# Kernel optimization log

Hardware: AMD Instinct MI355X
Metric: run time of the kernel (lower is better)

## Reference

```python
import jax, jax.numpy as jnp
import numpy as np

B = 8192
K = 64
GLOBAL = 16384  # static size of global index space (fill_max of teacher_indices)
TEMPERATURE = 2.0


def setup_inputs() -> dict:
    key = jax.random.key(0)
    k1, k2, k3 = jax.random.split(key, 3)
    student_logits = jax.random.normal(k1, (B, B), dtype=jnp.float32)
    teacher_scores = jax.random.uniform(k2, (B, K), dtype=jnp.float32)
    batch_indices = jnp.arange(B, dtype=jnp.int32)
    teacher_indices = jax.random.randint(k3, (B, K), 0, GLOBAL, dtype=jnp.int32)
    return {
        "student_logits": student_logits,
        "teacher_scores": teacher_scores,
        "batch_indices": batch_indices,
        "teacher_indices": teacher_indices,
    }


def reference(student_logits, teacher_scores, batch_indices, teacher_indices):
    b = student_logits.shape[0]
    # global -> local mapping table (-1 = not in batch). Static size GLOBAL.
    g2l = jnp.full((GLOBAL,), -1, dtype=jnp.int32).at[batch_indices].set(
        jnp.arange(b, dtype=jnp.int32))
    clamped = jnp.clip(teacher_indices, 0, GLOBAL - 1)
    local_pos = g2l[clamped]                       # [B, K]
    valid = local_pos >= 0
    # invalid entries -> column index b, dropped by scatter mode='drop'
    cols = jnp.where(valid, local_pos, b)
    rows = jnp.broadcast_to(jnp.arange(b, dtype=jnp.int32)[:, None], cols.shape)
    target_probs = jnp.zeros((b, b), dtype=student_logits.dtype)
    target_probs = target_probs.at[rows, cols].set(teacher_scores, mode="drop")
    diag = jnp.arange(b)
    target_probs = target_probs.at[diag, diag].set(1.0)
    row_sums = jnp.clip(target_probs.sum(axis=1, keepdims=True), 1e-8, None)
    target_probs = target_probs / row_sums
    student_log_probs = jax.nn.log_softmax(student_logits / TEMPERATURE, axis=1)
    # KLDivLoss(reduction='batchmean'): sum_t t*(log t - logp) / B, 0 where t==0
    safe_log_t = jnp.log(jnp.where(target_probs > 0, target_probs, 1.0))
    pointwise = jnp.where(target_probs > 0,
                          target_probs * (safe_log_t - student_log_probs), 0.0)
    loss = pointwise.sum() / b
    return loss * (TEMPERATURE ** 2)
```

## Files before the change

### kernel.cpp

```cpp
#include <hip/hip_runtime.h>
#include <math.h>

#define NB 8192
#define NK 64
#define NGLOBAL 16384
#define INV_T 0.5f
#define C_EXP2 0.72134752044448170f

#if defined(__has_builtin)
#if __has_builtin(__builtin_amdgcn_exp2f)
#define EXP2(x) __builtin_amdgcn_exp2f(x)
#endif
#endif
#ifndef EXP2
#define EXP2(x) exp2f(x)
#endif


__global__ __launch_bounds__(256) void row_loss_kernel(
    const float* __restrict__ S,
    const float* __restrict__ tscore,
    const int* __restrict__ tindex,
    const int* __restrict__ bidx,
    float* __restrict__ row_out)
{
    const int row = blockIdx.x;
    const int t = threadIdx.x;
    const float* __restrict__ Srow = S + (size_t)row * NB;
    const float4* rp = reinterpret_cast<const float4*>(Srow);

    float4 v[8];
#pragma unroll
    for (int i = 0; i < 8; ++i) v[i] = rp[i * 256 + t];

    int gi = 0; float sc = 0.f;
    if (t < NK) {
        gi = tindex[(size_t)row * NK + t];
        sc = tscore[(size_t)row * NK + t];
    }

    asm volatile("" ::: "memory");

    float s0 = 0.f, s1 = 0.f, s2 = 0.f, s3 = 0.f;
#pragma unroll
    for (int i = 0; i < 8; ++i) {
        s0 += EXP2(v[i].x * C_EXP2);
        s1 += EXP2(v[i].y * C_EXP2);
        s2 += EXP2(v[i].z * C_EXP2);
        s3 += EXP2(v[i].w * C_EXP2);
    }
    float s = (s0 + s1) + (s2 + s3);
#pragma unroll
    for (int off = 32; off >= 1; off >>= 1) s += __shfl_xor(s, off);
    __shared__ float sred[4];
    if ((t & 63) == 0) sred[t >> 6] = s;
    __syncthreads();

    if (t >= NK) return;

    gi = min(max(gi, 0), NGLOBAL - 1);
    const int col_s = min(gi, NB - 1);
    float gl_spec = Srow[col_s];
    float gd      = Srow[row];
    int   probe   = bidx[col_s];
    asm volatile("" ::: "memory");

    const float lse = __logf((sred[0] + sred[1]) + (sred[2] + sred[3]));

#pragma unroll
    for (int k = 1; k < NK; ++k) {
        int ck = __shfl(gi, k);
        if (t < k && ck == gi) sc = -1.f;
    }
    const bool valid = (gi < NB) && (probe == gi) && (gi != row);
    const bool live  = valid && (sc >= 0.f);

    float part = live ? sc : 0.f;
#pragma unroll
    for (int off = 32; off >= 1; off >>= 1) part += __shfl_xor(part, off);
    const float row_sum = 1.0f + part;

    float gl = valid ? gl_spec : gd;
    float term = 0.f;
    if (live && sc > 0.f) {
        float tv = sc / row_sum;
        float logp = fmaf(gl, INV_T, -lse);
        term = tv * (__logf(tv) - logp);
    }
    if (t == 0) {
        float td = 1.0f / row_sum;
        float logp = fmaf(gd, INV_T, -lse);
        term += td * (__logf(td) - logp);
    }
#pragma unroll
    for (int off = 32; off >= 1; off >>= 1) term += __shfl_xor(term, off);
    if (t == 0) row_out[row] = term;
}

__global__ __launch_bounds__(1024) void final_reduce_kernel(
    const float* __restrict__ row_out, float* __restrict__ out) {
    const int t = threadIdx.x;
    const float4* rp = reinterpret_cast<const float4*>(row_out);
    float4 w0 = rp[t], w1 = rp[1024 + t];
    asm volatile("" ::: "memory");
    double acc = (double)((w0.x + w0.y) + (w0.z + w0.w))
               + (double)((w1.x + w1.y) + (w1.z + w1.w));
#pragma unroll
    for (int off = 32; off >= 1; off >>= 1) acc += __shfl_xor(acc, off);
    __shared__ double sd[16];
    if ((t & 63) == 0) sd[t >> 6] = acc;
    __syncthreads();
    if (t == 0) {
        double total = 0.0;
#pragma unroll
        for (int i = 0; i < 16; ++i) total += sd[i];
        out[0] = (float)(total / (double)NB * 4.0);
    }
}

extern "C" void kernel_launch(void* const* d_in, const int* in_sizes, int n_in,
                              void* d_out, int out_size, void* d_ws, size_t ws_size,
                              hipStream_t stream) {
    const float* S      = (const float*)d_in[0];
    const float* tscore = (const float*)d_in[1];
    const int*   bidx   = (const int*)d_in[2];
    const int*   tindex = (const int*)d_in[3];
    float* out = (float*)d_out;

    float* row_out = (float*)d_ws;

    row_loss_kernel<<<NB, 256, 0, stream>>>(S, tscore, tindex, bidx, row_out);
    final_reduce_kernel<<<1, 1024, 0, stream>>>(row_out, out);
}
```

Measured before the change: 50.59 us.

## Process each row with a single wavefront and double-buffered loads

Each row is now handled by one 64-lane wavefront instead of a 256-thread block. The row is read in four chunks with two register buffers so loads of the next chunk overlap the exp-sum of the current one. This removes the shared-memory reduction, the __syncthreads, and the three idle warps in the tail phase. In exchange each wave carries more serial work and has less memory-level parallelism per row, so the kernel leans on occupancy across many blocks to hide latency.

```diff
diff --git a/kernel.cpp b/kernel.cpp
--- a/kernel.cpp
+++ b/kernel.cpp
@@ -17,7 +17,22 @@
 #endif
 
 
-__global__ __launch_bounds__(256) void row_loss_kernel(
+#define LOAD8(buf, c)                                                     \
+    _Pragma("unroll")                                                     \
+    for (int j = 0; j < 8; ++j) buf[j] = rp[(c) * 512 + j * 64 + lane];
+
+#define SUM8(buf)                                                         \
+    _Pragma("unroll")                                                     \
+    for (int j = 0; j < 8; ++j) {                                         \
+        s0 += EXP2(buf[j].x * C_EXP2);                                    \
+        s1 += EXP2(buf[j].y * C_EXP2);                                    \
+        s2 += EXP2(buf[j].z * C_EXP2);                                    \
+        s3 += EXP2(buf[j].w * C_EXP2);                                    \
+    }
+
+#define PIN() asm volatile("" ::: "memory")
+
+__global__ __launch_bounds__(64) void row_loss_kernel(
     const float* __restrict__ S,
     const float* __restrict__ tscore,
     const int* __restrict__ tindex,
@@ -25,52 +40,37 @@
     float* __restrict__ row_out)
 {
     const int row = blockIdx.x;
-    const int t = threadIdx.x;
+    const int lane = threadIdx.x;
     const float* __restrict__ Srow = S + (size_t)row * NB;
     const float4* rp = reinterpret_cast<const float4*>(Srow);
 
-    float4 v[8];
-#pragma unroll
-    for (int i = 0; i < 8; ++i) v[i] = rp[i * 256 + t];
+    int   gi = tindex[(size_t)row * NK + lane];
+    float sc = tscore[(size_t)row * NK + lane];
 
-    int gi = 0; float sc = 0.f;
-    if (t < NK) {
-        gi = tindex[(size_t)row * NK + t];
-        sc = tscore[(size_t)row * NK + t];
-    }
+    float4 va[8], vb[8];
+    float s0 = 0.f, s1 = 0.f, s2 = 0.f, s3 = 0.f;
+    LOAD8(va, 0); PIN();
+    LOAD8(vb, 1); PIN(); SUM8(va);
+    LOAD8(va, 2); PIN(); SUM8(vb);
+    LOAD8(vb, 3); PIN(); SUM8(va);
+    SUM8(vb);
 
-    asm volatile("" ::: "memory");
-
-    float s0 = 0.f, s1 = 0.f, s2 = 0.f, s3 = 0.f;
-#pragma unroll
-    for (int i = 0; i < 8; ++i) {
-        s0 += EXP2(v[i].x * C_EXP2);
-        s1 += EXP2(v[i].y * C_EXP2);
-        s2 += EXP2(v[i].z * C_EXP2);
-        s3 += EXP2(v[i].w * C_EXP2);
-    }
     float s = (s0 + s1) + (s2 + s3);
 #pragma unroll
     for (int off = 32; off >= 1; off >>= 1) s += __shfl_xor(s, off);
-    __shared__ float sred[4];
-    if ((t & 63) == 0) sred[t >> 6] = s;
-    __syncthreads();
-
-    if (t >= NK) return;
+    const float lse = __logf(s);
 
     gi = min(max(gi, 0), NGLOBAL - 1);
     const int col_s = min(gi, NB - 1);
     float gl_spec = Srow[col_s];
     float gd      = Srow[row];
     int   probe   = bidx[col_s];
-    asm volatile("" ::: "memory");
-
-    const float lse = __logf((sred[0] + sred[1]) + (sred[2] + sred[3]));
+    PIN();
 
 #pragma unroll
     for (int k = 1; k < NK; ++k) {
         int ck = __shfl(gi, k);
-        if (t < k && ck == gi) sc = -1.f;
+        if (lane < k && ck == gi) sc = -1.f;
     }
     const bool valid = (gi < NB) && (probe == gi) && (gi != row);
     const bool live  = valid && (sc >= 0.f);
@@ -87,14 +87,14 @@
         float logp = fmaf(gl, INV_T, -lse);
         term = tv * (__logf(tv) - logp);
     }
-    if (t == 0) {
+    if (lane == 0) {
         float td = 1.0f / row_sum;
         float logp = fmaf(gd, INV_T, -lse);
         term += td * (__logf(td) - logp);
     }
 #pragma unroll
     for (int off = 32; off >= 1; off >>= 1) term += __shfl_xor(term, off);
-    if (t == 0) row_out[row] = term;
+    if (lane == 0) row_out[row] = term;
 }
 
 __global__ __launch_bounds__(1024) void final_reduce_kernel(
@@ -129,6 +129,6 @@
 
     float* row_out = (float*)d_ws;
 
-    row_loss_kernel<<<NB, 256, 0, stream>>>(S, tscore, tindex, bidx, row_out);
+    row_loss_kernel<<<NB, 64, 0, stream>>>(S, tscore, tindex, bidx, row_out);
     final_reduce_kernel<<<1, 1024, 0, stream>>>(row_out, out);
 }
```

Result: slower. 52.10 us (+3.0%).
